# Kernel optimization log

Measured on AMD Instinct MI355X. Metric: run time of the kernel, lower is better.

Reference implementation:

```python
import jax, jax.numpy as jnp
import numpy as np

B, L, T = 32, 300, 12           # batch, enc_len, dec_len
H, E = 256, 128                 # hidden_size, input_size (embed dim)
V, OOV, NPR, UNK = 50000, 30, 6, 1  # vocab, max_article_oov, nprons, unk_id


def setup_inputs() -> dict:
    key = jax.random.key(0)
    ks = jax.random.split(key, 32)
    s = 0.05
    n = lambda k, sh: jax.random.normal(k, sh, jnp.float32) * s
    return {
        'enc_states': jax.random.normal(ks[0], (B, L, 2 * H), jnp.float32),
        'enc_h0': jax.random.normal(ks[1], (B, H), jnp.float32),
        'enc_c0': jax.random.normal(ks[2], (B, H), jnp.float32),
        'enc_mask': jnp.zeros((B, L), bool),
        'article_inds': jax.random.randint(ks[3], (B, L), 0, V + OOV),
        'dec_input': jax.random.randint(ks[4], (B, T), 0, V),
        'targets': jax.random.randint(ks[5], (B, T), 0, V + OOV),
        'dec_lens': jnp.full((B,), float(T), jnp.float32),
        'dec_mask': jnp.ones((B, T), jnp.float32),
        'embed': n(ks[6], (V, E)),
        'W_ih': n(ks[7], (E, 4 * H)),
        'W_hh': n(ks[8], (H, 4 * H)),
        'b_lstm': n(ks[9], (4 * H,)),
        'Wh_w': n(ks[10], (2 * H, 2 * H)), 'Wh_b': n(ks[11], (2 * H,)),
        'Ws_w': n(ks[12], (H, 2 * H)), 'Ws_b': n(ks[13], (2 * H,)),
        'v_w': n(ks[14], (2 * H,)), 'v_b': n(ks[15], ()),
        'wh_w': n(ks[16], (2 * H, 3)), 'wh_b': n(ks[17], (3,)),
        'ws_w': n(ks[18], (H, 3)), 'ws_b': n(ks[19], (3,)),
        'wx_w': n(ks[20], (E, 3)), 'wx_b': n(ks[21], (3,)),
        'wc_w': n(ks[22], (H, 3)), 'wc_b': n(ks[23], (3,)),
        'Vout_w': n(ks[24], (3 * H, V)), 'Vout_b': n(ks[25], (V,)),
    }


def reference(enc_states, enc_h0, enc_c0, enc_mask, article_inds, dec_input,
              targets, dec_lens, dec_mask, embed, W_ih, W_hh, b_lstm,
              Wh_w, Wh_b, Ws_w, Ws_b, v_w, v_b, wh_w, wh_b, ws_w, ws_b,
              wx_w, wx_b, wc_w, wc_b, Vout_w, Vout_b):
    x = embed[dec_input]                                  # [B,T,E]

    def lstm_step(carry, xt):
        h, c = carry
        g = xt @ W_ih + h @ W_hh + b_lstm                 # [B,4H], torch order i,f,g,o
        i, f, gg, o = jnp.split(g, 4, axis=-1)
        c = jax.nn.sigmoid(f) * c + jax.nn.sigmoid(i) * jnp.tanh(gg)
        h = jax.nn.sigmoid(o) * jnp.tanh(c)
        return (h, c), h

    _, hs = jax.lax.scan(lstm_step, (enc_h0, enc_c0), jnp.swapaxes(x, 0, 1))
    hidden = jnp.swapaxes(hs, 0, 1)                       # [B,T,H]

    # Bahdanau attention, batched over all decode steps
    enc_proj = enc_states @ Wh_w + Wh_b                   # [B,L,2H]
    dec_proj = hidden @ Ws_w + Ws_b                       # [B,T,2H]
    e = jnp.tanh(enc_proj[:, None] + dec_proj[:, :, None]) @ v_w + v_b  # [B,T,L]
    e = jnp.where(enc_mask[:, None, :], -jnp.inf, e)
    attn = jax.nn.softmax(e, axis=-1)                     # [B,T,L]
    context = jnp.einsum('btl,ble->bte', attn, enc_states)  # [B,T,2H]

    p_vocab = jax.nn.softmax(jnp.concatenate([hidden, context], -1) @ Vout_w + Vout_b, axis=-1)
    sw = (context @ wh_w + wh_b) + (hidden @ ws_w + ws_b) + (x @ wx_w + wx_b) \
         + (enc_h0 @ wc_w + wc_b)[:, None]                # [B,T,3]
    p_switch = jax.nn.softmax(sw, axis=-1)

    vocab_ids = jnp.arange(V)
    p_gen = jnp.where(vocab_ids < V - NPR, p_switch[..., 0:1], p_switch[..., 1:2])  # [B,T,V]
    weighted = p_gen * p_vocab
    combined = jnp.concatenate([weighted, jnp.zeros((B, T, OOV), weighted.dtype)], -1)
    wattn = p_switch[..., 2:3] * attn                     # [B,T,L]
    # scatter-add copy distribution into extended vocab (per batch row)
    combined = jax.vmap(lambda cv, idx, w: cv.at[:, idx].add(w))(combined, article_inds, wattn)

    out = jnp.take_along_axis(combined, targets[..., None], axis=-1)[..., 0]  # [B,T]
    out = jnp.where(targets == UNK, 1.0, out)
    loss = (-jnp.log(out) * dec_mask).sum(1) / dec_lens   # [B]
    return loss
```

## Files before the change

### kernel.cpp

```cpp
#include <hip/hip_runtime.h>
#include <hip/hip_bf16.h>
#include <math.h>

#define BB 32
#define LL 300
#define TT 12
#define HH 256
#define EE 128
#define VV 50000
#define OOV 30
#define NPR 6
#define UNK 1
#define H2 512
#define H3 768
#define H4 1024
#define BT (BB*TT)
#define NVB 391
#define KSTEPS 24
#define NT32P (196*8)

#define OFF_X        0
#define OFF_HID      (OFF_X + BT*EE)
#define OFF_ENCP     (OFF_HID + BT*HH)
#define OFF_DECP     (OFF_ENCP + BB*LL*H2)
#define OFF_ATTN     (OFF_DECP + BT*H2)
#define OFF_S        (OFF_ATTN + BT*LL)
#define OFF_PSW      (OFF_S + BT*H3)
#define OFF_COPY     (OFF_PSW + BT*3)
#define OFF_TLOGIT   (OFF_COPY + BT)
#define OFF_PMAX     (OFF_TLOGIT + BT)
#define OFF_PSUM     (OFF_PMAX + BT*NVB)
#define OFF_NLL      (OFF_PSUM + BT*NVB)
#define OFF_APACK    (OFF_NLL + BT)
#define OFF_XW       (OFF_APACK + BT*H3/2)
#define OFF_WHH      (OFF_XW + BT*H4)
#define OFF_HFRAG    (OFF_WHH + 131072)
#define OFF_BAR      (OFF_HFRAG + 8192)
#define OFF_BPACK    (OFF_BAR + 64)
#define BPACK_SHORTS ((size_t)NT32P*24*2*64*8)
#define WS_NEEDED_BYTES ((size_t)(OFF_BPACK)*4 + BPACK_SHORTS*2)
#define OFF_APENC (OFF_BPACK)
#define OFF_APHID (OFF_APENC + 2457600)
#define OFF_APX   (OFF_APHID + 49152)
#define OFF_BWIH  (OFF_APX + 24576)
#define OFF_BWHW  (OFF_BWIH + 65536)
#define OFF_BWSW  (OFF_BWHW + 131072)

typedef __attribute__((ext_vector_type(8))) short short8;
typedef __attribute__((ext_vector_type(16))) float floatx16;

__device__ __forceinline__ short f2bf(float f) {
    __hip_bfloat16 h = __float2bfloat16(f);
    return *reinterpret_cast<short*>(&h);
}
__device__ __forceinline__ float bf2f(short s) {
    unsigned int u = ((unsigned int)(unsigned short)s) << 16;
    return __uint_as_float(u);
}
__device__ __forceinline__ float sigm(float x) { return 1.f/(1.f + expf(-x)); }

__global__ __launch_bounds__(256) void k_embed(
    const float* __restrict__ embed, const int* __restrict__ dec_input,
    float* __restrict__ x_out)
{
    int i = blockIdx.x*256 + threadIdx.x;
    int bt = i >> 5;
    int e4 = i & 31;
    int tok = dec_input[bt];
    reinterpret_cast<float4*>(x_out)[(size_t)bt*32 + e4] =
        reinterpret_cast<const float4*>(embed)[(size_t)tok*32 + e4];
}

__global__ __launch_bounds__(256) void k_apack(
    const float* __restrict__ A, short* __restrict__ Ap, int MT, int K_)
{
    int s = blockIdx.x*256 + threadIdx.x;
    int l = s & 63;
    int ks = (s >> 6) & 1;
    int rest = s >> 7;
    int mt = rest % MT;
    int kstep = rest / MT;
    int row = mt*32 + (l & 31);
    int kb = kstep*32 + ks*16 + ((l >> 5) << 3);
    const float4* src = reinterpret_cast<const float4*>(&A[(size_t)row*K_ + kb]);
    float4 a = src[0], b = src[1];
    short8 v;
    v[0]=f2bf(a.x); v[1]=f2bf(a.y); v[2]=f2bf(a.z); v[3]=f2bf(a.w);
    v[4]=f2bf(b.x); v[5]=f2bf(b.y); v[6]=f2bf(b.z); v[7]=f2bf(b.w);
    *reinterpret_cast<short8*>(Ap + (size_t)s*8) = v;
}

__global__ __launch_bounds__(256) void k_wpack(
    const float* __restrict__ W, short* __restrict__ Bp, int KS, int N_)
{
    int s = blockIdx.x*256 + threadIdx.x;
    int l = s & 63;
    int ks = (s >> 6) & 1;
    int rest = s >> 7;
    int kstep = rest % KS;
    int ct = rest / KS;
    int col = ct*32 + (l & 31);
    int kb = kstep*32 + ks*16 + ((l >> 5) << 3);
    short8 v;
    #pragma unroll
    for (int j = 0; j < 8; ++j) v[j] = f2bf(W[(size_t)(kb + j)*N_ + col]);
    *reinterpret_cast<short8*>(Bp + (size_t)s*8) = v;
}

__global__ __launch_bounds__(512) void k_gemm_mfma(
    const short* __restrict__ Apack, const short* __restrict__ Bpack,
    const float* __restrict__ bias, float* __restrict__ C,
    int N_, int MT, int KS)
{
    int bm = blockIdx.x, nb = blockIdx.y;
    int t = threadIdx.x;
    int wid = t >> 6, lane = t & 63;
    int wave_m = wid >> 2, wave_n = wid & 3;
    int mt0 = bm*6 + wave_m*3;
    int ct = nb*4 + wave_n;

    const short8* ap = reinterpret_cast<const short8*>(Apack);
    const short8* bp = reinterpret_cast<const short8*>(Bpack);

    floatx16 acc[3];
    #pragma unroll
    for (int mi = 0; mi < 3; ++mi)
        #pragma unroll
        for (int r = 0; r < 16; ++r) acc[mi][r] = 0.f;

    short8 Ba0, Ba1, Bb0, Bb1;
    short8 Fa[6], Fb[6];

#define LOADB(B0, B1, kst) do { \
    B0 = bp[(size_t)(((ct*KS + (kst))*2 + 0)*64 + lane)]; \
    B1 = bp[(size_t)(((ct*KS + (kst))*2 + 1)*64 + lane)]; \
} while (0)
#define LOADA(F, kst) do { \
    _Pragma("unroll") \
    for (int mi = 0; mi < 3; ++mi) { \
        F[mi]   = ap[(size_t)((((kst)*MT + (mt0 + mi))*2 + 0)*64 + lane)]; \
        F[3+mi] = ap[(size_t)((((kst)*MT + (mt0 + mi))*2 + 1)*64 + lane)]; \
    } \
} while (0)
#define STEP(B0, B1, F) do { \
    _Pragma("unroll") \
    for (int mi = 0; mi < 3; ++mi) \
        acc[mi] = __builtin_amdgcn_mfma_f32_32x32x16_bf16(F[mi], B0, acc[mi], 0, 0, 0); \
    _Pragma("unroll") \
    for (int mi = 0; mi < 3; ++mi) \
        acc[mi] = __builtin_amdgcn_mfma_f32_32x32x16_bf16(F[3+mi], B1, acc[mi], 0, 0, 0); \
} while (0)

    LOADB(Ba0, Ba1, 0); LOADA(Fa, 0);
    LOADB(Bb0, Bb1, 1); LOADA(Fb, 1);
    for (int k = 0; k < KS; k += 2) {
        STEP(Ba0, Ba1, Fa);
        if (k + 2 < KS) { LOADB(Ba0, Ba1, k+2); LOADA(Fa, k+2); }
        STEP(Bb0, Bb1, Fb);
        if (k + 3 < KS) { LOADB(Bb0, Bb1, k+3); LOADA(Fb, k+3); }
    }
#undef LOADB
#undef LOADA
#undef STEP

    int col = ct*32 + (lane & 31);
    float bias_v = bias[col];
    int rsub = 4*(lane >> 5);
    #pragma unroll
    for (int mi = 0; mi < 3; ++mi) {
        int rowg0 = bm*192 + wave_m*96 + mi*32 + rsub;
        #pragma unroll
        for (int r = 0; r < 16; ++r) {
            int rowg = rowg0 + (r & 3) + 8*(r >> 2);
            C[(size_t)rowg*N_ + col] = acc[mi][r] + bias_v;
        }
    }
}

__global__ __launch_bounds__(256) void k_gemm_bias(
    const float* __restrict__ A, const float* __restrict__ Wm,
    const float* __restrict__ bias, float* __restrict__ C, int N_, int K_)
{
    __shared__ float As[64][17];
    __shared__ __align__(16) float Bs[16][128];
    int bm = blockIdx.x*64, bn = blockIdx.y*128;
    int tid = threadIdx.x, tr = tid >> 4, tc = tid & 15;
    float acc[4][8] = {};
    for (int k0 = 0; k0 < K_; k0 += 16) {
        for (int i = tid; i < 64*16; i += 256) { int r = i >> 4, c = i & 15; As[r][c] = A[(size_t)(bm+r)*K_ + k0 + c]; }
        for (int i = tid; i < 16*128; i += 256) { int r = i >> 7, c = i & 127; Bs[r][c] = Wm[(size_t)(k0+r)*N_ + bn + c]; }
        __syncthreads();
        #pragma unroll
        for (int kk = 0; kk < 16; ++kk) {
            float a0 = As[tr*4+0][kk], a1 = As[tr*4+1][kk], a2 = As[tr*4+2][kk], a3 = As[tr*4+3][kk];
            const float4* bpx = reinterpret_cast<const float4*>(&Bs[kk][tc*8]);
            float4 q0 = bpx[0], q1 = bpx[1];
            float bb[8] = {q0.x,q0.y,q0.z,q0.w,q1.x,q1.y,q1.z,q1.w};
            #pragma unroll
            for (int j = 0; j < 8; ++j) {
                acc[0][j] += a0*bb[j]; acc[1][j] += a1*bb[j];
                acc[2][j] += a2*bb[j]; acc[3][j] += a3*bb[j];
            }
        }
        __syncthreads();
    }
    for (int i = 0; i < 4; ++i) {
        int r = bm + tr*4 + i;
        for (int j = 0; j < 8; ++j) {
            int c = bn + tc*8 + j;
            C[(size_t)r*N_ + c] = acc[i][j] + bias[c];
        }
    }
}

__global__ __launch_bounds__(256) void k_whh_pack(
    const float* __restrict__ Whh, short* __restrict__ wp)
{
    int s = blockIdx.x*256 + threadIdx.x;
    int l = s & 63;
    int kstep = (s >> 6) & 15;
    int ct_l = (s >> 10) & 7;
    int q = s >> 13;
    int col = (ct_l >> 1)*256 + q*64 + (ct_l & 1)*32 + (l & 31);
    int kb = kstep*16 + ((l >> 5) << 3);
    short8 v;
    #pragma unroll
    for (int j = 0; j < 8; ++j) v[j] = f2bf(Whh[(size_t)(kb + j)*H4 + col]);
    *reinterpret_cast<short8*>(wp + (size_t)s*8) = v;
}

__global__ __launch_bounds__(256) void k_init(
    const float* __restrict__ h0, short* __restrict__ hbuf0,
    unsigned int* __restrict__ bar)
{
    int gid = blockIdx.x*256 + threadIdx.x;
    int r = gid >> 8;
    int hidx = gid & 255;
    int kstep = hidx >> 4;
    int kk = hidx & 15;
    int l = ((kk >> 3) << 5) + r;
    hbuf0[(size_t)(kstep*64 + l)*8 + (kk & 7)] = f2bf(h0[r*HH + hidx]);
    if (blockIdx.x == 0 && threadIdx.x < 64) bar[threadIdx.x] = 0u;
}

__global__ __launch_bounds__(512) void k_lstm5(
    const float* __restrict__ xw, const short* __restrict__ whhp,
    const float* __restrict__ c0, short* __restrict__ hbuf,
    unsigned int* __restrict__ bar, float* __restrict__ hid_out)
{
    __shared__ short wlds[8*16*64*8];
    __shared__ short g_lds[32][256];
    __shared__ float c_lds[32][64];
    int tid = threadIdx.x, wid = tid >> 6, lane = tid & 63;
    int q = blockIdx.x;

    {
        const short8* wp8 = reinterpret_cast<const short8*>(whhp);
        for (int i = tid; i < 8192; i += 512)
            *reinterpret_cast<short8*>(&wlds[i*8]) = wp8[(size_t)q*8192 + i];
    }
    for (int i = tid; i < 32*64; i += 512) {
        int b = i >> 6, jj = i & 63;
        c_lds[b][jj] = c0[b*HH + q*64 + jj];
    }
    __syncthreads();

    for (int t = 0; t < TT; ++t) {
        const short* hcur = hbuf + (size_t)(t & 1)*8192;
        short* hnxt = hbuf + (size_t)((t + 1) & 1)*8192;

        floatx16 acc;
        #pragma unroll
        for (int r = 0; r < 16; ++r) acc[r] = 0.f;
        #pragma unroll
        for (int kstep = 0; kstep < 16; ++kstep) {
            short8 af = *reinterpret_cast<const short8*>(&hcur[(size_t)(kstep*64 + lane)*8]);
            short8 bf = *reinterpret_cast<const short8*>(&wlds[((wid*16 + kstep)*64 + lane)*8]);
            acc = __builtin_amdgcn_mfma_f32_32x32x16_bf16(af, bf, acc, 0, 0, 0);
        }
        int gcol = (wid >> 1)*256 + q*64 + (wid & 1)*32 + (lane & 31);
        int lcol = wid*32 + (lane & 31);
        #pragma unroll
        for (int r = 0; r < 16; ++r) {
            int row = (r & 3) + 8*(r >> 2) + 4*(lane >> 5);
            g_lds[row][lcol] = f2bf(acc[r] + xw[(size_t)(row*TT + t)*H4 + gcol]);
        }
        __syncthreads();
        for (int i = tid; i < 2048; i += 512) {
            int b = i >> 6, jj = i & 63;
            float gi = bf2f(g_lds[b][((0*2 + (jj>>5))<<5) + (jj & 31)]);
            float gf = bf2f(g_lds[b][((1*2 + (jj>>5))<<5) + (jj & 31)]);
            float gg = bf2f(g_lds[b][((2*2 + (jj>>5))<<5) + (jj & 31)]);
            float go = bf2f(g_lds[b][((3*2 + (jj>>5))<<5) + (jj & 31)]);
            float c = sigm(gf)*c_lds[b][jj] + sigm(gi)*tanhf(gg);
            float h = sigm(go)*tanhf(c);
            c_lds[b][jj] = c;
            int hidx = q*64 + jj;
            hid_out[(size_t)(b*TT + t)*HH + hidx] = h;
            int kk = hidx & 15;
            int l2 = ((kk >> 3) << 5) + b;
            hnxt[(size_t)((hidx >> 4)*64 + l2)*8 + (kk & 7)] = f2bf(h);
        }
        __threadfence();
        __syncthreads();
        if (tid == 0) {
            atomicAdd(&bar[t], 1u);
            while (atomicAdd(&bar[t], 0u) < 4u) __builtin_amdgcn_s_sleep(2);
        }
        __syncthreads();
        __threadfence();
    }
}

__global__ __launch_bounds__(256) void k_e(
    const float* __restrict__ enc_proj, const float* __restrict__ dec_proj,
    const float* __restrict__ v_w, const float* __restrict__ v_b,
    const unsigned char* __restrict__ enc_mask, float* __restrict__ e_out)
{
    int b = blockIdx.x, lbase = blockIdx.y*4;
    __shared__ float decp[TT*H2];
    int tid = threadIdx.x;
    for (int i = tid; i < TT*H2; i += 256) decp[i] = dec_proj[(size_t)b*TT*H2 + i];
    __syncthreads();
    int wave = tid >> 6, lane = tid & 63;
    int l = lbase + wave;
    const float* er = &enc_proj[(size_t)(b*LL + l)*H2];
    float ep[8], vw[8];
    #pragma unroll
    for (int k = 0; k < 8; ++k) { int e = lane + 64*k; ep[k] = er[e]; vw[k] = v_w[e]; }
    float vb = v_b[0];
    bool masked = enc_mask[b*LL + l] != 0;
    for (int t = 0; t < TT; ++t) {
        float acc = 0.f;
        #pragma unroll
        for (int k = 0; k < 8; ++k) {
            int e = lane + 64*k;
            acc += vw[k] * tanhf(ep[k] + decp[t*H2 + e]);
        }
        #pragma unroll
        for (int off = 32; off; off >>= 1) acc += __shfl_xor(acc, off);
        if (lane == 0)
            e_out[(size_t)(b*TT + t)*LL + l] = masked ? -INFINITY : (acc + vb);
    }
}

__global__ __launch_bounds__(256) void k_softmax_ctx(
    float* __restrict__ attn, const float* __restrict__ enc_states,
    const float* __restrict__ hidden, float* __restrict__ s_out)
{
    int bt = blockIdx.x, b = bt / TT, tid = threadIdx.x;
    __shared__ float a[LL];
    __shared__ float red[256];
    float m = -INFINITY;
    for (int l = tid; l < LL; l += 256) m = fmaxf(m, attn[(size_t)bt*LL + l]);
    red[tid] = m; __syncthreads();
    for (int s = 128; s; s >>= 1) { if (tid < s) red[tid] = fmaxf(red[tid], red[tid+s]); __syncthreads(); }
    m = red[0]; __syncthreads();
    float sum = 0.f;
    for (int l = tid; l < LL; l += 256) { float w = expf(attn[(size_t)bt*LL + l] - m); a[l] = w; sum += w; }
    red[tid] = sum; __syncthreads();
    for (int s = 128; s; s >>= 1) { if (tid < s) red[tid] += red[tid+s]; __syncthreads(); }
    float inv = 1.0f / red[0];
    __syncthreads();
    for (int l = tid; l < LL; l += 256) { float w = a[l]*inv; a[l] = w; attn[(size_t)bt*LL + l] = w; }
    __syncthreads();
    for (int c = tid; c < H2; c += 256) {
        float acc = 0.f;
        const float* es = &enc_states[(size_t)b*LL*H2 + c];
        for (int l = 0; l < LL; ++l) acc += a[l] * es[(size_t)l*H2];
        s_out[(size_t)bt*H3 + HH + c] = acc;
    }
    for (int c = tid; c < HH; c += 256) s_out[(size_t)bt*H3 + c] = hidden[(size_t)bt*HH + c];
}

__global__ __launch_bounds__(64) void k_switch_copy(
    const float* __restrict__ s, const float* __restrict__ x,
    const float* __restrict__ enc_h0,
    const float* __restrict__ wh_w, const float* __restrict__ wh_b,
    const float* __restrict__ ws_w, const float* __restrict__ ws_b,
    const float* __restrict__ wx_w, const float* __restrict__ wx_b,
    const float* __restrict__ wc_w, const float* __restrict__ wc_b,
    const int* __restrict__ article_inds, const int* __restrict__ targets,
    const float* __restrict__ attn, float* __restrict__ psw, float* __restrict__ copysc)
{
    int bt = blockIdx.x, b = bt / TT, lane = threadIdx.x;
    float s0 = 0.f, s1 = 0.f, s2 = 0.f;
    const float* ctx = &s[(size_t)bt*H3 + HH];
    const float* hid = &s[(size_t)bt*H3];
    for (int k = lane; k < H2; k += 64) { float v = ctx[k]; s0 += v*wh_w[k*3]; s1 += v*wh_w[k*3+1]; s2 += v*wh_w[k*3+2]; }
    for (int k = lane; k < HH; k += 64) { float v = hid[k]; s0 += v*ws_w[k*3]; s1 += v*ws_w[k*3+1]; s2 += v*ws_w[k*3+2]; }
    for (int k = lane; k < EE; k += 64) { float v = x[(size_t)bt*EE + k]; s0 += v*wx_w[k*3]; s1 += v*wx_w[k*3+1]; s2 += v*wx_w[k*3+2]; }
    for (int k = lane; k < HH; k += 64) { float v = enc_h0[b*HH + k]; s0 += v*wc_w[k*3]; s1 += v*wc_w[k*3+1]; s2 += v*wc_w[k*3+2]; }
    #pragma unroll
    for (int off = 32; off; off >>= 1) {
        s0 += __shfl_xor(s0, off); s1 += __shfl_xor(s1, off); s2 += __shfl_xor(s2, off);
    }
    if (lane == 0) {
        s0 += wh_b[0] + ws_b[0] + wx_b[0] + wc_b[0];
        s1 += wh_b[1] + ws_b[1] + wx_b[1] + wc_b[1];
        s2 += wh_b[2] + ws_b[2] + wx_b[2] + wc_b[2];
        float mm = fmaxf(s0, fmaxf(s1, s2));
        float e0 = expf(s0-mm), e1 = expf(s1-mm), e2 = expf(s2-mm);
        float inv = 1.f/(e0+e1+e2);
        psw[bt*3+0] = e0*inv; psw[bt*3+1] = e1*inv; psw[bt*3+2] = e2*inv;
    }
    int tgt = targets[bt];
    float cs = 0.f;
    for (int l = lane; l < LL; l += 64)
        if (article_inds[b*LL + l] == tgt) cs += attn[(size_t)bt*LL + l];
    #pragma unroll
    for (int off = 32; off; off >>= 1) cs += __shfl_xor(cs, off);
    if (lane == 0) copysc[bt] = cs;
}

__global__ __launch_bounds__(256) void k_bpack(
    const float* __restrict__ Wm, short* __restrict__ Bp)
{
    __shared__ short tile[32][264];
    int kstep = blockIdx.x, cblk = blockIdx.y;
    int tid = threadIdx.x;
    int cbase = cblk*256;
    for (int i = tid; i < 32*64; i += 256) {
        int r = i >> 6, c4 = i & 63;
        int col = cbase + c4*4;
        float4 v = make_float4(0.f,0.f,0.f,0.f);
        if (col < VV)
            v = *reinterpret_cast<const float4*>(&Wm[(size_t)(kstep*32 + r)*VV + col]);
        tile[r][c4*4+0] = f2bf(v.x); tile[r][c4*4+1] = f2bf(v.y);
        tile[r][c4*4+2] = f2bf(v.z); tile[r][c4*4+3] = f2bf(v.w);
    }
    __syncthreads();
    int wave = tid >> 6, l = tid & 63;
    #pragma unroll
    for (int it = 0; it < 4; ++it) {
        int fid = wave*4 + it;
        int ct_l = fid >> 1, ks = fid & 1;
        int rbase = ks*16 + ((l >> 5) << 3);
        int c = ct_l*32 + (l & 31);
        short8 v;
        #pragma unroll
        for (int j = 0; j < 8; ++j) v[j] = tile[rbase + j][c];
        size_t ct_g = (size_t)cblk*8 + ct_l;
        *reinterpret_cast<short8*>(&Bp[(((ct_g*24 + kstep)*2 + ks)*64 + l)*8]) = v;
    }
}

__global__ __launch_bounds__(512) void k_big_packed(
    const short* __restrict__ Apack, const short* __restrict__ Bp,
    const float* __restrict__ bias, const int* __restrict__ targets,
    float* __restrict__ psum, float* __restrict__ tlogit)
{
    __shared__ float pv_l[192][4];
    int bm = blockIdx.x, nvb = blockIdx.y;
    int bn = nvb * 128;
    int t = threadIdx.x;
    int wid = t >> 6, lane = t & 63;
    int wave_m = wid >> 2, wave_n = wid & 3;
    size_t ct_g = (size_t)nvb*4 + wave_n;
    int colB = bn + wave_n*32 + (lane & 31);
    bool colOK = colB < VV;
    int mt0 = bm*6 + wave_m*3;

    const short8* ap = reinterpret_cast<const short8*>(Apack);
    const short8* bp8 = reinterpret_cast<const short8*>(Bp);

    floatx16 acc[3];
    #pragma unroll
    for (int mi = 0; mi < 3; ++mi)
        #pragma unroll
        for (int r = 0; r < 16; ++r) acc[mi][r] = 0.f;

    short8 Ba0, Ba1, Bb0, Bb1;
    short8 Fa[6], Fb[6];

#define LOADB(B0, B1, kst) do { \
    B0 = bp8[((ct_g*24 + (kst))*2 + 0)*64 + lane]; \
    B1 = bp8[((ct_g*24 + (kst))*2 + 1)*64 + lane]; \
} while (0)
#define LOADA(F, kst) do { \
    _Pragma("unroll") \
    for (int mi = 0; mi < 3; ++mi) { \
        F[mi]   = ap[(size_t)(((kst)*12 + (mt0 + mi))*2 + 0)*64 + lane]; \
        F[3+mi] = ap[(size_t)(((kst)*12 + (mt0 + mi))*2 + 1)*64 + lane]; \
    } \
} while (0)
#define STEP(B0, B1, F) do { \
    _Pragma("unroll") \
    for (int mi = 0; mi < 3; ++mi) \
        acc[mi] = __builtin_amdgcn_mfma_f32_32x32x16_bf16(F[mi], B0, acc[mi], 0, 0, 0); \
    _Pragma("unroll") \
    for (int mi = 0; mi < 3; ++mi) \
        acc[mi] = __builtin_amdgcn_mfma_f32_32x32x16_bf16(F[3+mi], B1, acc[mi], 0, 0, 0); \
} while (0)

    LOADB(Ba0, Ba1, 0); LOADA(Fa, 0);
    LOADB(Bb0, Bb1, 1); LOADA(Fb, 1);
    for (int k = 0; k < KSTEPS; k += 2) {
        STEP(Ba0, Ba1, Fa);
        if (k + 2 < KSTEPS) { LOADB(Ba0, Ba1, k+2); LOADA(Fa, k+2); }
        STEP(Bb0, Bb1, Fb);
        if (k + 3 < KSTEPS) { LOADB(Bb0, Bb1, k+3); LOADA(Fb, k+3); }
    }
#undef LOADB
#undef LOADA
#undef STEP

    float bias_v = colOK ? bias[colB] : 0.f;
    int rsub = 4*(lane >> 5);
    #pragma unroll
    for (int mi = 0; mi < 3; ++mi) {
        #pragma unroll
        for (int r = 0; r < 16; ++r) {
            int row_l = wave_m*96 + mi*32 + rsub + (r & 3) + 8*(r >> 2);
            int rowg = bm*192 + row_l;
            float logit = acc[mi][r] + bias_v;
            if (colOK && colB == targets[rowg]) tlogit[rowg] = logit;
            float e = colOK ? expf(logit) : 0.f;
            #pragma unroll
            for (int msk = 16; msk; msk >>= 1) e += __shfl_xor(e, msk);
            if ((lane & 31) == 0) pv_l[row_l][wave_n] = e;
        }
    }
    __syncthreads();
    if (t < 192) {
        float ss = pv_l[t][0] + pv_l[t][1] + pv_l[t][2] + pv_l[t][3];
        int rowg = bm*192 + t;
        psum[(size_t)rowg*NVB + nvb] = ss;
    }
}

__global__ __launch_bounds__(512) void k_big(
    const short* __restrict__ Apack, const float* __restrict__ Wm,
    const float* __restrict__ bias, const int* __restrict__ targets,
    float* __restrict__ psum, float* __restrict__ tlogit)
{
    __shared__ float pv_l[192][4];
    int bm = blockIdx.x, nvb = blockIdx.y;
    int bn = nvb * 128;
    int t = threadIdx.x;
    int wid = t >> 6, lane = t & 63;
    int wave_m = wid >> 2, wave_n = wid & 3;
    int colB = bn + wave_n*32 + (lane & 31);
    int kOff = (lane >> 5) << 3;
    bool colOK = colB < VV;
    int mt0 = bm*6 + wave_m*3;
    const short8* ap = reinterpret_cast<const short8*>(Apack);
    floatx16 acc[3];
    #pragma unroll
    for (int mi = 0; mi < 3; ++mi)
        #pragma unroll
        for (int r = 0; r < 16; ++r) acc[mi][r] = 0.f;
    float Bq0a[8], Bq1a[8], Bq0b[8], Bq1b[8];
    short8 Fa[6], Fb[6];
#define LOADB(Q0, Q1, kst) do { \
    int kb_ = (kst)*32 + kOff; \
    _Pragma("unroll") \
    for (int j = 0; j < 8; ++j) Q0[j] = colOK ? Wm[(size_t)(kb_ + j)*VV + colB] : 0.f; \
    _Pragma("unroll") \
    for (int j = 0; j < 8; ++j) Q1[j] = colOK ? Wm[(size_t)(kb_ + 16 + j)*VV + colB] : 0.f; \
} while (0)
#define LOADA(F, kst) do { \
    _Pragma("unroll") \
    for (int mi = 0; mi < 3; ++mi) { \
        F[mi]   = ap[(size_t)(((kst)*12 + (mt0 + mi))*2 + 0)*64 + lane]; \
        F[3+mi] = ap[(size_t)(((kst)*12 + (mt0 + mi))*2 + 1)*64 + lane]; \
    } \
} while (0)
#define STEP(Q0, Q1, F) do { \
    short8 b0_, b1_; \
    _Pragma("unroll") \
    for (int j = 0; j < 8; ++j) { b0_[j] = f2bf(Q0[j]); b1_[j] = f2bf(Q1[j]); } \
    _Pragma("unroll") \
    for (int mi = 0; mi < 3; ++mi) \
        acc[mi] = __builtin_amdgcn_mfma_f32_32x32x16_bf16(F[mi], b0_, acc[mi], 0, 0, 0); \
    _Pragma("unroll") \
    for (int mi = 0; mi < 3; ++mi) \
        acc[mi] = __builtin_amdgcn_mfma_f32_32x32x16_bf16(F[3+mi], b1_, acc[mi], 0, 0, 0); \
} while (0)
    LOADB(Bq0a, Bq1a, 0); LOADA(Fa, 0);
    LOADB(Bq0b, Bq1b, 1); LOADA(Fb, 1);
    for (int k = 0; k < KSTEPS; k += 2) {
        STEP(Bq0a, Bq1a, Fa);
        if (k + 2 < KSTEPS) { LOADB(Bq0a, Bq1a, k+2); LOADA(Fa, k+2); }
        STEP(Bq0b, Bq1b, Fb);
        if (k + 3 < KSTEPS) { LOADB(Bq0b, Bq1b, k+3); LOADA(Fb, k+3); }
    }
#undef LOADB
#undef LOADA
#undef STEP
    float bias_v = colOK ? bias[colB] : 0.f;
    int rsub = 4*(lane >> 5);
    #pragma unroll
    for (int mi = 0; mi < 3; ++mi) {
        #pragma unroll
        for (int r = 0; r < 16; ++r) {
            int row_l = wave_m*96 + mi*32 + rsub + (r & 3) + 8*(r >> 2);
            int rowg = bm*192 + row_l;
            float logit = acc[mi][r] + bias_v;
            if (colOK && colB == targets[rowg]) tlogit[rowg] = logit;
            float e = colOK ? expf(logit) : 0.f;
            #pragma unroll
            for (int msk = 16; msk; msk >>= 1) e += __shfl_xor(e, msk);
            if ((lane & 31) == 0) pv_l[row_l][wave_n] = e;
        }
    }
    __syncthreads();
    if (t < 192) {
        float ss = pv_l[t][0] + pv_l[t][1] + pv_l[t][2] + pv_l[t][3];
        int rowg = bm*192 + t;
        psum[(size_t)rowg*NVB + nvb] = ss;
    }
}

__global__ __launch_bounds__(64) void k_lsum(
    const float* __restrict__ psum,
    const float* __restrict__ tlogit, const int* __restrict__ targets,
    const float* __restrict__ psw, const float* __restrict__ copysc,
    const float* __restrict__ dec_mask, float* __restrict__ nll)
{
    int pair = blockIdx.x, lane = threadIdx.x;
    float s = 0.f;
    for (int j = lane; j < NVB; j += 64) s += psum[(size_t)pair*NVB + j];
    #pragma unroll
    for (int off = 32; off; off >>= 1) s += __shfl_xor(s, off);
    if (lane == 0) {
        int tgt = targets[pair];
        float outv;
        if (tgt == UNK) outv = 1.0f;
        else {
            float base = 0.f;
            if (tgt < VV) {
                float pvv = expf(tlogit[pair]) / s;
                float pg = (tgt < VV - NPR) ? psw[pair*3] : psw[pair*3+1];
                base = pg * pvv;
            }
            outv = base + psw[pair*3+2] * copysc[pair];
        }
        outv = fmaxf(outv, 1e-38f);
        nll[pair] = -logf(outv) * dec_mask[pair];
    }
}

__global__ __launch_bounds__(64) void k_final(
    const float* __restrict__ nll, const float* __restrict__ dec_lens, float* __restrict__ out)
{
    int b = threadIdx.x;
    if (b < BB) {
        float a = 0.f;
        for (int t = 0; t < TT; ++t) a += nll[b*TT + t];
        out[b] = a / dec_lens[b];
    }
}

extern "C" void kernel_launch(void* const* d_in, const int* in_sizes, int n_in,
                              void* d_out, int out_size, void* d_ws, size_t ws_size,
                              hipStream_t stream)
{
    const float* enc_states = (const float*)d_in[0];
    const float* enc_h0     = (const float*)d_in[1];
    const float* enc_c0     = (const float*)d_in[2];
    const unsigned char* enc_mask = (const unsigned char*)d_in[3];
    const int* article_inds = (const int*)d_in[4];
    const int* dec_input    = (const int*)d_in[5];
    const int* targets      = (const int*)d_in[6];
    const float* dec_lens   = (const float*)d_in[7];
    const float* dec_mask   = (const float*)d_in[8];
    const float* embed      = (const float*)d_in[9];
    const float* W_ih       = (const float*)d_in[10];
    const float* W_hh       = (const float*)d_in[11];
    const float* b_lstm     = (const float*)d_in[12];
    const float* Wh_w = (const float*)d_in[13]; const float* Wh_b = (const float*)d_in[14];
    const float* Ws_w = (const float*)d_in[15]; const float* Ws_b = (const float*)d_in[16];
    const float* v_w  = (const float*)d_in[17]; const float* v_b  = (const float*)d_in[18];
    const float* wh_w = (const float*)d_in[19]; const float* wh_b = (const float*)d_in[20];
    const float* ws_w = (const float*)d_in[21]; const float* ws_b = (const float*)d_in[22];
    const float* wx_w = (const float*)d_in[23]; const float* wx_b = (const float*)d_in[24];
    const float* wc_w = (const float*)d_in[25]; const float* wc_b = (const float*)d_in[26];
    const float* Vout_w = (const float*)d_in[27]; const float* Vout_b = (const float*)d_in[28];

    float* ws = (float*)d_ws;
    float* x_buf   = ws + OFF_X;
    float* hid     = ws + OFF_HID;
    float* encp    = ws + OFF_ENCP;
    float* decp    = ws + OFF_DECP;
    float* attn    = ws + OFF_ATTN;
    float* s_buf   = ws + OFF_S;
    float* psw     = ws + OFF_PSW;
    float* copysc  = ws + OFF_COPY;
    float* tlogit  = ws + OFF_TLOGIT;
    float* psum    = ws + OFF_PSUM;
    float* nll     = ws + OFF_NLL;
    short* apack   = (short*)(ws + OFF_APACK);
    float* xw      = ws + OFF_XW;
    short* whhp    = (short*)(ws + OFF_WHH);
    short* hbuf    = (short*)(ws + OFF_HFRAG);
    unsigned int* bar = (unsigned int*)(ws + OFF_BAR);
    short* bpack   = (short*)(ws + OFF_BPACK);
    short* apenc   = (short*)(ws + OFF_APENC);
    short* aphid   = (short*)(ws + OFF_APHID);
    short* apx     = (short*)(ws + OFF_APX);
    short* bwih    = (short*)(ws + OFF_BWIH);
    short* bwhw    = (short*)(ws + OFF_BWHW);
    short* bwsw    = (short*)(ws + OFF_BWSW);
    float* out     = (float*)d_out;

    bool use_pack = ws_size >= WS_NEEDED_BYTES;

    k_embed<<<dim3(BT*EE/4/256), dim3(256), 0, stream>>>(embed, dec_input, x_buf);

    if (use_pack) {
        k_apack<<<dim3(BT*EE/8/256), dim3(256), 0, stream>>>(x_buf, apx, 12, EE);
        k_wpack<<<dim3(EE*H4/8/256), dim3(256), 0, stream>>>(W_ih, bwih, EE/32, H4);
        k_gemm_mfma<<<dim3(BT/192, H4/128), dim3(512), 0, stream>>>(apx, bwih, b_lstm, xw, H4, BT/32, EE/32);
    } else {
        k_gemm_bias<<<dim3(BT/64, H4/128), dim3(256), 0, stream>>>(x_buf, W_ih, b_lstm, xw, H4, EE);
    }
    k_whh_pack<<<dim3(128), dim3(256), 0, stream>>>(W_hh, whhp);
    k_init<<<dim3(32), dim3(256), 0, stream>>>(enc_h0, hbuf, bar);
    k_lstm5<<<dim3(4), dim3(512), 0, stream>>>(xw, whhp, enc_c0, hbuf, bar, hid);

    if (use_pack) {
        k_apack<<<dim3(BB*LL*H2/8/256), dim3(256), 0, stream>>>(enc_states, apenc, BB*LL/32, H2);
        k_wpack<<<dim3(H2*H2/8/256), dim3(256), 0, stream>>>(Wh_w, bwhw, H2/32, H2);
        k_gemm_mfma<<<dim3(BB*LL/192, H2/128), dim3(512), 0, stream>>>(apenc, bwhw, Wh_b, encp, H2, BB*LL/32, H2/32);
        k_apack<<<dim3(BT*HH/8/256), dim3(256), 0, stream>>>(hid, aphid, 12, HH);
        k_wpack<<<dim3(HH*H2/8/256), dim3(256), 0, stream>>>(Ws_w, bwsw, HH/32, H2);
        k_gemm_mfma<<<dim3(BT/192, H2/128), dim3(512), 0, stream>>>(aphid, bwsw, Ws_b, decp, H2, BT/32, HH/32);
    } else {
        k_gemm_bias<<<dim3(BB*LL/64, H2/128), dim3(256), 0, stream>>>(enc_states, Wh_w, Wh_b, encp, H2, H2);
        k_gemm_bias<<<dim3(BT/64, H2/128), dim3(256), 0, stream>>>(hid, Ws_w, Ws_b, decp, H2, HH);
    }
    k_e<<<dim3(BB, LL/4), dim3(256), 0, stream>>>(encp, decp, v_w, v_b, enc_mask, attn);
    k_softmax_ctx<<<dim3(BT), dim3(256), 0, stream>>>(attn, enc_states, hid, s_buf);
    k_switch_copy<<<dim3(BT), dim3(64), 0, stream>>>(s_buf, x_buf, enc_h0,
        wh_w, wh_b, ws_w, ws_b, wx_w, wx_b, wc_w, wc_b,
        article_inds, targets, attn, psw, copysc);
    k_apack<<<dim3(BT*H3/8/256), dim3(256), 0, stream>>>(s_buf, apack, 12, H3);
    if (use_pack) {
        k_bpack<<<dim3(24, 196), dim3(256), 0, stream>>>(Vout_w, bpack);
        k_big_packed<<<dim3(2, NVB), dim3(512), 0, stream>>>(apack, bpack, Vout_b, targets, psum, tlogit);
    } else {
        k_big<<<dim3(2, NVB), dim3(512), 0, stream>>>(apack, Vout_w, Vout_b, targets, psum, tlogit);
    }
    k_lsum<<<dim3(BT), dim3(64), 0, stream>>>(psum, tlogit, targets, psw, copysc, dec_mask, nll);
    k_final<<<dim3(1), dim3(64), 0, stream>>>(nll, dec_lens, out);
}
```

Measured before the change: 359.7 us.

## Fuse Vout weight packing into vocab GEMM with async global-to-LDS staging

Removes the separate k_bpack pass that converted the fp32 Vout_w into a packed bf16 buffer. The vocab GEMM now streams fp32 weight tiles straight into double-buffered LDS with global_load_lds and converts them to bf16 while building fragments. Each block also covers all 384 rows instead of 192, so every weight tile is read once. The cost is one barrier per k-step, per-element LDS reads with conversion, and a grid of 391 blocks of 512 threads at one block per CU.

Measured after the change: 363.7 us. No clear change (+1.1%).

```diff
diff --git a/kernel.cpp b/kernel.cpp
--- a/kernel.cpp
+++ b/kernel.cpp
@@ -59,6 +59,12 @@
 }
 __device__ __forceinline__ float sigm(float x) { return 1.f/(1.f + expf(-x)); }
 
+__device__ __forceinline__ void gload_lds16(const float* g, float* l) {
+    __builtin_amdgcn_global_load_lds(
+        (const __attribute__((address_space(1))) void*)g,
+        (__attribute__((address_space(3))) void*)l, 16, 0, 0);
+}
+
 __global__ __launch_bounds__(256) void k_embed(
     const float* __restrict__ embed, const int* __restrict__ dec_input,
     float* __restrict__ x_out)
@@ -107,7 +113,7 @@
     *reinterpret_cast<short8*>(Bp + (size_t)s*8) = v;
 }
 
-__global__ __launch_bounds__(512) void k_gemm_mfma(
+__global__ __launch_bounds__(512, 1) void k_gemm_mfma(
     const short* __restrict__ Apack, const short* __restrict__ Bpack,
     const float* __restrict__ bias, float* __restrict__ C,
     int N_, int MT, int KS)
@@ -413,119 +419,86 @@
     if (lane == 0) copysc[bt] = cs;
 }
 
-__global__ __launch_bounds__(256) void k_bpack(
-    const float* __restrict__ Wm, short* __restrict__ Bp)
-{
-    __shared__ short tile[32][264];
-    int kstep = blockIdx.x, cblk = blockIdx.y;
-    int tid = threadIdx.x;
-    int cbase = cblk*256;
-    for (int i = tid; i < 32*64; i += 256) {
-        int r = i >> 6, c4 = i & 63;
-        int col = cbase + c4*4;
-        float4 v = make_float4(0.f,0.f,0.f,0.f);
-        if (col < VV)
-            v = *reinterpret_cast<const float4*>(&Wm[(size_t)(kstep*32 + r)*VV + col]);
-        tile[r][c4*4+0] = f2bf(v.x); tile[r][c4*4+1] = f2bf(v.y);
-        tile[r][c4*4+2] = f2bf(v.z); tile[r][c4*4+3] = f2bf(v.w);
-    }
-    __syncthreads();
-    int wave = tid >> 6, l = tid & 63;
-    #pragma unroll
-    for (int it = 0; it < 4; ++it) {
-        int fid = wave*4 + it;
-        int ct_l = fid >> 1, ks = fid & 1;
-        int rbase = ks*16 + ((l >> 5) << 3);
-        int c = ct_l*32 + (l & 31);
-        short8 v;
-        #pragma unroll
-        for (int j = 0; j < 8; ++j) v[j] = tile[rbase + j][c];
-        size_t ct_g = (size_t)cblk*8 + ct_l;
-        *reinterpret_cast<short8*>(&Bp[(((ct_g*24 + kstep)*2 + ks)*64 + l)*8]) = v;
-    }
-}
-
-__global__ __launch_bounds__(512) void k_big_packed(
-    const short* __restrict__ Apack, const short* __restrict__ Bp,
+__global__ __launch_bounds__(512, 1) void k_big_fused(
+    const short* __restrict__ Apack, const float* __restrict__ Wm,
     const float* __restrict__ bias, const int* __restrict__ targets,
     float* __restrict__ psum, float* __restrict__ tlogit)
 {
-    __shared__ float pv_l[192][4];
-    int bm = blockIdx.x, nvb = blockIdx.y;
+    __shared__ float btile[2][32*128];
+    __shared__ float pv_l[384][4];
+    int nvb = blockIdx.x;
     int bn = nvb * 128;
     int t = threadIdx.x;
     int wid = t >> 6, lane = t & 63;
     int wave_m = wid >> 2, wave_n = wid & 3;
-    size_t ct_g = (size_t)nvb*4 + wave_n;
-    int colB = bn + wave_n*32 + (lane & 31);
-    bool colOK = colB < VV;
-    int mt0 = bm*6 + wave_m*3;
+
+    int gcol = bn + ((lane & 31) << 2);
+    bool gOK = gcol <= (VV - 4);
+    int goff = gOK ? gcol : 0;
 
     const short8* ap = reinterpret_cast<const short8*>(Apack);
-    const short8* bp8 = reinterpret_cast<const short8*>(Bp);
-
-    floatx16 acc[3];
-    #pragma unroll
-    for (int mi = 0; mi < 3; ++mi)
+
+    floatx16 acc[6];
+    #pragma unroll
+    for (int mi = 0; mi < 6; ++mi)
         #pragma unroll
         for (int r = 0; r < 16; ++r) acc[mi][r] = 0.f;
 
-    short8 Ba0, Ba1, Bb0, Bb1;
-    short8 Fa[6], Fb[6];
-
-#define LOADB(B0, B1, kst) do { \
-    B0 = bp8[((ct_g*24 + (kst))*2 + 0)*64 + lane]; \
-    B1 = bp8[((ct_g*24 + (kst))*2 + 1)*64 + lane]; \
-} while (0)
-#define LOADA(F, kst) do { \
-    _Pragma("unroll") \
-    for (int mi = 0; mi < 3; ++mi) { \
-        F[mi]   = ap[(size_t)(((kst)*12 + (mt0 + mi))*2 + 0)*64 + lane]; \
-        F[3+mi] = ap[(size_t)(((kst)*12 + (mt0 + mi))*2 + 1)*64 + lane]; \
+#define STAGE(buf, kst) do { \
+    _Pragma("unroll") \
+    for (int rr = 0; rr < 2; ++rr) { \
+        int row = rr*16 + wid*2 + (lane >> 5); \
+        const float* g = Wm + (size_t)((kst)*32 + row)*VV + goff; \
+        float* l = &btile[buf][(rr*16 + wid*2)*128]; \
+        gload_lds16(g, l); \
     } \
 } while (0)
-#define STEP(B0, B1, F) do { \
-    _Pragma("unroll") \
-    for (int mi = 0; mi < 3; ++mi) \
-        acc[mi] = __builtin_amdgcn_mfma_f32_32x32x16_bf16(F[mi], B0, acc[mi], 0, 0, 0); \
-    _Pragma("unroll") \
-    for (int mi = 0; mi < 3; ++mi) \
-        acc[mi] = __builtin_amdgcn_mfma_f32_32x32x16_bf16(F[3+mi], B1, acc[mi], 0, 0, 0); \
-} while (0)
-
-    LOADB(Ba0, Ba1, 0); LOADA(Fa, 0);
-    LOADB(Bb0, Bb1, 1); LOADA(Fb, 1);
-    for (int k = 0; k < KSTEPS; k += 2) {
-        STEP(Ba0, Ba1, Fa);
-        if (k + 2 < KSTEPS) { LOADB(Ba0, Ba1, k+2); LOADA(Fa, k+2); }
-        STEP(Bb0, Bb1, Fb);
-        if (k + 3 < KSTEPS) { LOADB(Bb0, Bb1, k+3); LOADA(Fb, k+3); }
-    }
-#undef LOADB
-#undef LOADA
-#undef STEP
-
-    float bias_v = colOK ? bias[colB] : 0.f;
+
+    STAGE(0, 0);
+    __syncthreads();
+
+    int cb = wave_n*32 + (lane & 31);
+    int k0r = (lane >> 5) << 3;
+    for (int k = 0; k < KSTEPS; ++k) {
+        int cur = k & 1;
+        if (k + 1 < KSTEPS) STAGE(cur ^ 1, k + 1);
+        short8 bf0, bf1;
+        #pragma unroll
+        for (int j = 0; j < 8; ++j) bf0[j] = f2bf(btile[cur][(k0r + j)*128 + cb]);
+        #pragma unroll
+        for (int j = 0; j < 8; ++j) bf1[j] = f2bf(btile[cur][(16 + k0r + j)*128 + cb]);
+        #pragma unroll
+        for (int mi = 0; mi < 6; ++mi) {
+            short8 af0 = ap[(size_t)((k*12 + (wave_m*6 + mi))*2 + 0)*64 + lane];
+            acc[mi] = __builtin_amdgcn_mfma_f32_32x32x16_bf16(af0, bf0, acc[mi], 0, 0, 0);
+            short8 af1 = ap[(size_t)((k*12 + (wave_m*6 + mi))*2 + 1)*64 + lane];
+            acc[mi] = __builtin_amdgcn_mfma_f32_32x32x16_bf16(af1, bf1, acc[mi], 0, 0, 0);
+        }
+        __syncthreads();
+    }
+#undef STAGE
+
+    int colW = bn + wave_n*32 + (lane & 31);
+    bool colOK = colW < VV;
+    float bias_v = colOK ? bias[colW] : 0.f;
     int rsub = 4*(lane >> 5);
     #pragma unroll
-    for (int mi = 0; mi < 3; ++mi) {
+    for (int mi = 0; mi < 6; ++mi) {
         #pragma unroll
         for (int r = 0; r < 16; ++r) {
-            int row_l = wave_m*96 + mi*32 + rsub + (r & 3) + 8*(r >> 2);
-            int rowg = bm*192 + row_l;
+            int rowg = wave_m*192 + mi*32 + rsub + (r & 3) + 8*(r >> 2);
             float logit = acc[mi][r] + bias_v;
-            if (colOK && colB == targets[rowg]) tlogit[rowg] = logit;
+            if (colOK && colW == targets[rowg]) tlogit[rowg] = logit;
             float e = colOK ? expf(logit) : 0.f;
             #pragma unroll
             for (int msk = 16; msk; msk >>= 1) e += __shfl_xor(e, msk);
-            if ((lane & 31) == 0) pv_l[row_l][wave_n] = e;
+            if ((lane & 31) == 0) pv_l[rowg][wave_n] = e;
         }
     }
     __syncthreads();
-    if (t < 192) {
+    if (t < 384) {
         float ss = pv_l[t][0] + pv_l[t][1] + pv_l[t][2] + pv_l[t][3];
-        int rowg = bm*192 + t;
-        psum[(size_t)rowg*NVB + nvb] = ss;
+        psum[(size_t)t*NVB + nvb] = ss;
     }
 }
 
@@ -695,7 +668,6 @@
     short* whhp    = (short*)(ws + OFF_WHH);
     short* hbuf    = (short*)(ws + OFF_HFRAG);
     unsigned int* bar = (unsigned int*)(ws + OFF_BAR);
-    short* bpack   = (short*)(ws + OFF_BPACK);
     short* apenc   = (short*)(ws + OFF_APENC);
     short* aphid   = (short*)(ws + OFF_APHID);
     short* apx     = (short*)(ws + OFF_APX);
@@ -737,8 +709,7 @@
         article_inds, targets, attn, psw, copysc);
     k_apack<<<dim3(BT*H3/8/256), dim3(256), 0, stream>>>(s_buf, apack, 12, H3);
     if (use_pack) {
-        k_bpack<<<dim3(24, 196), dim3(256), 0, stream>>>(Vout_w, bpack);
-        k_big_packed<<<dim3(2, NVB), dim3(512), 0, stream>>>(apack, bpack, Vout_b, targets, psum, tlogit);
+        k_big_fused<<<dim3(NVB), dim3(512), 0, stream>>>(apack, Vout_w, Vout_b, targets, psum, tlogit);
     } else {
         k_big<<<dim3(2, NVB), dim3(512), 0, stream>>>(apack, Vout_w, Vout_b, targets, psum, tlogit);
     }
```
